# Kernel tuning notes

Hardware: AMD Instinct MI355X
Metric: run time of the kernel (lower is better)

The kernel has to match this reference:

```python
import jax, jax.numpy as jnp
import numpy as np

DIM = 256
NUM_HEADS = 4
HEAD_DIM = DIM // NUM_HEADS


def setup_inputs() -> dict:
    key = jax.random.key(0)
    ks = jax.random.split(key, 8)
    B, N, C = 4, 2048, DIM
    x = jax.random.normal(ks[0], (B, N, C), dtype=jnp.float32)
    R = jax.random.normal(ks[1], (B, 3, 3), dtype=jnp.float32)
    P = jax.random.normal(ks[2], (N, 3), dtype=jnp.float32)
    s = 1.0 / np.sqrt(C)
    qkv_w = jax.random.normal(ks[3], (3 * C, C), dtype=jnp.float32) * s
    qkv_b = jax.random.normal(ks[4], (3 * C,), dtype=jnp.float32) * 0.02
    proj_w = jax.random.normal(ks[5], (C, C), dtype=jnp.float32) * s
    proj_b = jax.random.normal(ks[6], (C,), dtype=jnp.float32) * 0.02
    pos_scale = jnp.asarray(1.0, dtype=jnp.float32)
    return {"x": x, "R": R, "P": P, "qkv_w": qkv_w, "qkv_b": qkv_b,
            "proj_w": proj_w, "proj_b": proj_b, "pos_scale": pos_scale}


def reference(x, R, P, qkv_w, qkv_b, proj_w, proj_b, pos_scale):
    B, N, C = x.shape
    H, D = NUM_HEADS, HEAD_DIM
    scale = D ** -0.5
    # qkv: (B,N,3C) -> (3,B,H,N,D)
    qkv = (x @ qkv_w.T + qkv_b).reshape(B, N, 3, H, D).transpose(2, 0, 3, 1, 4)
    q, k, v = qkv[0], qkv[1], qkv[2]
    # attention logits (B,H,N,N)
    attn = jnp.einsum('bhid,bhjd->bhij', q, k) * scale
    # positional bias: RP = (R @ P^T)^T -> (B,N,3); bias_ij = dot(RP_i, P_j)
    RP = jnp.einsum('bab,jb->bja', R, P) if False else jnp.einsum('bca,ja->bjc', jnp.swapaxes(R, 1, 2), P)
    RP = jnp.einsum('bcd,jd->bjc', R, P)  # (B,N,3): (R @ P.T).T
    bias = jnp.einsum('bik,jk->bij', RP, P)[:, None, :, :] * pos_scale  # (B,1,N,N) broadcast over heads
    attn = jax.nn.softmax(attn + bias, axis=-1)
    out = jnp.einsum('bhij,bhjd->bhid', attn, v)  # (B,H,N,D)
    out = out.transpose(0, 2, 1, 3).reshape(B, N, C)
    out = out @ proj_w.T + proj_b
    return out
```

## Files before the change

kernel.cpp:

```cpp
#include <hip/hip_runtime.h>
#include <hip/hip_bf16.h>

#define B_ 4
#define N_ 2048
#define C_ 256
#define H_ 4
#define D_ 64

typedef __attribute__((ext_vector_type(8))) short bf16x8;
typedef __attribute__((ext_vector_type(4))) float f32x4;

#define LOG2E 1.4426950408889634f

static __device__ inline unsigned short f2bf(float f) {
    unsigned u = __builtin_bit_cast(unsigned, f);
    unsigned r = (u + 0x7fffu + ((u >> 16) & 1u)) >> 16;
    return (unsigned short)r;
}
static __device__ inline float bf2f(unsigned short h) {
    unsigned u = ((unsigned)h) << 16;
    return __builtin_bit_cast(float, u);
}
static __device__ inline unsigned pack2(float a, float b) {
    __hip_bfloat162 h = __float22bfloat162_rn(make_float2(a, b));
    unsigned u;
    __builtin_memcpy(&u, &h, 4);
    return u;
}
static __device__ inline bf16x8 ld_frag(const unsigned short* p) {
    return __builtin_bit_cast(bf16x8, *(const uint4*)p);
}
static __device__ inline void gload_lds16(const unsigned short* g, unsigned short* l) {
    __builtin_amdgcn_global_load_lds(
        (const __attribute__((address_space(1))) unsigned int*)(g),
        (__attribute__((address_space(3))) unsigned int*)(l),
        16, 0, 0);
}
template<int CTRL>
static __device__ inline float fmax_dpp(float x) {
    int yi = __builtin_amdgcn_update_dpp(0, __builtin_bit_cast(int, x),
                                         CTRL, 0xf, 0xf, true);
    return fmaxf(x, __builtin_bit_cast(float, yi));
}

__global__ __launch_bounds__(256) void cvt_kernel(
    const float* __restrict__ x, const float* __restrict__ qkv_w,
    const float* __restrict__ proj_w, const float* __restrict__ Pm,
    unsigned short* __restrict__ xb, unsigned short* __restrict__ wqb,
    unsigned short* __restrict__ wpb, unsigned short* __restrict__ eb)
{
    const int bid = blockIdx.x, tid = threadIdx.x;
    if (bid >= 1152) {
        const int n = (bid - 1152) * 256 + tid;
        const float* pp = Pm + n * 3;
        float p0 = pp[0], p1 = pp[1], p2 = pp[2];
        unsigned u0 = f2bf(p0), u1 = f2bf(p1), u2 = f2bf(p2);
        unsigned v0 = f2bf(p0 - bf2f((unsigned short)u0));
        unsigned v1 = f2bf(p1 - bf2f((unsigned short)u1));
        unsigned v2 = f2bf(p2 - bf2f((unsigned short)u2));
        uint4 lo, hi;
        lo.x = u0 | (u1 << 16); lo.y = u2 | (v0 << 16);
        lo.z = v1 | (v2 << 16); lo.w = u0 | (u1 << 16);
        hi.x = u2; hi.y = 0u; hi.z = 0u; hi.w = 0u;
        *(uint4*)&eb[n * 16 + 0] = lo;
        *(uint4*)&eb[n * 16 + 8] = hi;
        return;
    }
    const float* s; unsigned short* d; int i;
    if (bid < 1024)      { s = x;      d = xb;  i = (bid * 256 + tid) * 8; }
    else if (bid < 1120) { s = qkv_w;  d = wqb; i = ((bid - 1024) * 256 + tid) * 8; }
    else                 { s = proj_w; d = wpb; i = ((bid - 1120) * 256 + tid) * 8; }
    float4 a = *(const float4*)(s + i);
    float4 b = *(const float4*)(s + i + 4);
    uint4 u;
    u.x = pack2(a.x, a.y); u.y = pack2(a.z, a.w);
    u.z = pack2(b.x, b.y); u.w = pack2(b.z, b.w);
    *(uint4*)(d + i) = u;
}

__global__ __launch_bounds__(256) void qkv_gemm(
    const unsigned short* __restrict__ xb, const unsigned short* __restrict__ wb,
    const float* __restrict__ bias, unsigned short* __restrict__ qb,
    unsigned short* __restrict__ kb, unsigned short* __restrict__ vt)
{
    __shared__ __align__(16) unsigned short As[128 * 40];
    __shared__ __align__(16) unsigned short Bs[128 * 40];
    const int m0 = blockIdx.x * 128, o0 = blockIdx.y * 128;
    const int tid = threadIdx.x;
    const int wave = tid >> 6, lane = tid & 63, quad = lane >> 4, l16 = lane & 15;
    const int wy = wave >> 1, wx = wave & 1;

    f32x4 acc[4][4];
    #pragma unroll
    for (int i = 0; i < 4; ++i)
        #pragma unroll
        for (int j = 0; j < 4; ++j) acc[i][j] = (f32x4){0.f, 0.f, 0.f, 0.f};

    const int srow = tid >> 1, soff = (tid & 1) * 16;

    for (int k0 = 0; k0 < 256; k0 += 32) {
        __syncthreads();
        {
            const unsigned short* sa = &xb[(size_t)(m0 + srow) * 256 + k0 + soff];
            const unsigned short* sb = &wb[(size_t)(o0 + srow) * 256 + k0 + soff];
            *(uint4*)&As[srow * 40 + soff + 0] = *(const uint4*)(sa + 0);
            *(uint4*)&As[srow * 40 + soff + 8] = *(const uint4*)(sa + 8);
            *(uint4*)&Bs[srow * 40 + soff + 0] = *(const uint4*)(sb + 0);
            *(uint4*)&Bs[srow * 40 + soff + 8] = *(const uint4*)(sb + 8);
        }
        __syncthreads();
        bf16x8 a[4], b[4];
        #pragma unroll
        for (int mt = 0; mt < 4; ++mt) a[mt] = ld_frag(&As[(wy * 64 + mt * 16 + l16) * 40 + quad * 8]);
        #pragma unroll
        for (int nt = 0; nt < 4; ++nt) b[nt] = ld_frag(&Bs[(wx * 64 + nt * 16 + l16) * 40 + quad * 8]);
        #pragma unroll
        for (int mt = 0; mt < 4; ++mt)
            #pragma unroll
            for (int nt = 0; nt < 4; ++nt)
                acc[mt][nt] = __builtin_amdgcn_mfma_f32_16x16x32_bf16(a[mt], b[nt], acc[mt][nt], 0, 0, 0);
    }

    const int sec = o0 + wx * 64;
    const int three = sec >> 8;
    const int h = (sec >> 6) & 3;
    const int b = m0 >> 11;
    float bv[4];
    #pragma unroll
    for (int nt = 0; nt < 4; ++nt) bv[nt] = bias[sec + nt * 16 + l16];

    if (three == 2) {
        const int n64 = (m0 + wy * 64) & 2047;
        const size_t bh64 = ((size_t)b * H_ + h) * 64;
        #pragma unroll
        for (int nt = 0; nt < 4; ++nt) {
            int d = nt * 16 + l16;
            #pragma unroll
            for (int r = 0; r < 4; ++r) {
                ushort4 v;
                v.x = f2bf(acc[0][nt][r] + bv[nt]);
                v.y = f2bf(acc[1][nt][r] + bv[nt]);
                v.z = f2bf(acc[2][nt][r] + bv[nt]);
                v.w = f2bf(acc[3][nt][r] + bv[nt]);
                *(ushort4*)&vt[(bh64 + d) * N_ + n64 + 16 * quad + 4 * r] = v;
            }
        }
    } else {
        unsigned short* dst = (three == 0) ? qb : kb;
        float sc = (three == 0) ? (0.125f * LOG2E) : 1.0f;
        #pragma unroll
        for (int mt = 0; mt < 4; ++mt)
            #pragma unroll
            for (int r = 0; r < 4; ++r) {
                int n = (m0 + wy * 64 + mt * 16 + quad * 4 + r) & 2047;
                size_t rowbase = (((size_t)b * H_ + h) * N_ + n) * D_;
                #pragma unroll
                for (int nt = 0; nt < 4; ++nt)
                    dst[rowbase + nt * 16 + l16] = f2bf((acc[mt][nt][r] + bv[nt]) * sc);
            }
    }
}

#define LDK 64

__global__ __launch_bounds__(256) void attn_kernel(
    const unsigned short* __restrict__ qb, const unsigned short* __restrict__ kb,
    const unsigned short* __restrict__ vt, const unsigned short* __restrict__ eb,
    const float* __restrict__ Rm, const float* __restrict__ Pm,
    const float* __restrict__ ps_ptr,
    unsigned short* __restrict__ Opart, float* __restrict__ ml)
{
    __shared__ __align__(16) unsigned short Ks[2][64 * LDK];
    __shared__ __align__(16) unsigned short Vs[64 * LDK];
    __shared__ __align__(16) unsigned short Ps[64 * LDK];

    const int bh = blockIdx.y;
    const int b = bh >> 2;
    const int i0 = blockIdx.x * 64;
    const int split = blockIdx.z;
    const int tid = threadIdx.x;
    const int wave = tid >> 6, lane = tid & 63;
    const int quad = lane >> 4, l16 = lane & 15;
    const int x7 = l16 & 7;
    const float ps = ps_ptr[0];

    const size_t base = (size_t)bh * N_ * D_;
    const unsigned short* qg = qb + base;
    const unsigned short* kg = kb + base;
    const unsigned short* vg = vt + base;

    const int jbeg = split * (N_ / 4);
    const int NT = (N_ / 4) / 64;

    const int rl = lane >> 3, sl = lane & 7;
    const int swz = (sl ^ rl) * 8;
    const unsigned short* kq = kg + (size_t)(jbeg + wave * 16 + rl) * D_ + swz;
    const unsigned short* vq = vg + (size_t)(wave * 16 + rl) * N_ + jbeg + swz;
    const unsigned short* ep = eb + (size_t)(jbeg + l16) * 16 + (quad & 1) * 8;

    {
        unsigned short* kd = &Ks[0][(wave * 16) * LDK];
        gload_lds16(kq,          kd);
        gload_lds16(kq + 8 * D_, kd + 8 * LDK);
        kq += 64 * D_;
    }
    bf16x8 ereg[4];
    #pragma unroll
    for (int t = 0; t < 4; ++t) ereg[t] = ld_frag(ep + t * 256);
    ep += 64 * 16;

    const int qrow = i0 + wave * 16 + l16;
    bf16x8 aq[3];
    #pragma unroll
    for (int ks = 0; ks < 2; ++ks)
        aq[ks] = ld_frag(&qg[(size_t)qrow * D_ + ks * 32 + quad * 8]);

    {
        float p0 = Pm[qrow * 3 + 0], p1 = Pm[qrow * 3 + 1], p2 = Pm[qrow * 3 + 2];
        float sc = ps * LOG2E;
        unsigned short ah[3], al[3];
        #pragma unroll
        for (int c = 0; c < 3; ++c) {
            float a = (Rm[b * 9 + c * 3 + 0] * p0 + Rm[b * 9 + c * 3 + 1] * p1
                     + Rm[b * 9 + c * 3 + 2] * p2) * sc;
            ah[c] = f2bf(a);
            al[c] = f2bf(a - bf2f(ah[c]));
        }
        bf16x8 e = (bf16x8){0,0,0,0,0,0,0,0};
        if (quad == 0) {
            e[0] = (short)ah[0]; e[1] = (short)ah[1]; e[2] = (short)ah[2];
            e[3] = (short)ah[0]; e[4] = (short)ah[1]; e[5] = (short)ah[2];
            e[6] = (short)al[0]; e[7] = (short)al[1];
        } else if (quad == 1) {
            e[0] = (short)al[2];
        }
        aq[2] = e;
    }

    const bf16x8 ones = (bf16x8){0x3F80,0x3F80,0x3F80,0x3F80,0x3F80,0x3F80,0x3F80,0x3F80};

    float m_run = -1e30f;
    f32x4 o_acc[4], lacc;
    #pragma unroll
    for (int t = 0; t < 4; ++t) o_acc[t] = (f32x4){0.f, 0.f, 0.f, 0.f};
    lacc = (f32x4){0.f, 0.f, 0.f, 0.f};

    for (int jt = 0; jt < NT; ++jt) {
        const int cur = jt & 1;
        const bool more = (jt + 1 < NT);

        asm volatile("s_waitcnt vmcnt(0)" ::: "memory");
        __builtin_amdgcn_s_barrier();
        __builtin_amdgcn_sched_barrier(0);

        bf16x8 enext[4];
        if (more) {
            #pragma unroll
            for (int t = 0; t < 4; ++t) enext[t] = ld_frag(ep + t * 256);
            ep += 64 * 16;
        }
        {
            unsigned short* vd = &Vs[(wave * 16) * LDK];
            gload_lds16(vq,          vd);
            gload_lds16(vq + 8 * N_, vd + 8 * LDK);
            vq += 64;
        }
        if (more) {
            unsigned short* kd = &Ks[cur ^ 1][(wave * 16) * LDK];
            gload_lds16(kq,          kd);
            gload_lds16(kq + 8 * D_, kd + 8 * LDK);
            kq += 64 * D_;
        }
        __builtin_amdgcn_sched_barrier(0);

        f32x4 s[4];
        __builtin_amdgcn_s_setprio(1);
        #pragma unroll
        for (int t = 0; t < 4; ++t) {
            const int rb = (l16 + 16 * t) * LDK;
            f32x4 c = {0.f, 0.f, 0.f, 0.f};
            #pragma unroll
            for (int ks = 0; ks < 2; ++ks) {
                bf16x8 bk = ld_frag(&Ks[cur][rb + (((ks * 4 + quad) ^ x7) * 8)]);
                c = __builtin_amdgcn_mfma_f32_16x16x32_bf16(aq[ks], bk, c, 0, 0, 0);
            }
            c = __builtin_amdgcn_mfma_f32_16x16x32_bf16(aq[2], ereg[t], c, 0, 0, 0);
            s[t] = c;
        }
        __builtin_amdgcn_s_setprio(0);
        if (more) {
            #pragma unroll
            for (int t = 0; t < 4; ++t) ereg[t] = enext[t];
        }

        float mt[4];
        #pragma unroll
        for (int t = 0; t < 4; ++t)
            mt[t] = fmaxf(fmaxf(s[t][0], s[t][1]), fmaxf(s[t][2], s[t][3]));
        float mx = fmaxf(fmaxf(mt[0], mt[1]), fmaxf(mt[2], mt[3]));
        mx = fmax_dpp<0xB1>(mx);
        mx = fmax_dpp<0x4E>(mx);
        mx = fmax_dpp<0x124>(mx);
        mx = fmax_dpp<0x128>(mx);

        if (__any(mx > m_run + 8.0f)) {
            float mnew = fmaxf(m_run, mx);
            float alpha = exp2f(m_run - mnew);
            #pragma unroll
            for (int t = 0; t < 4; ++t)
                #pragma unroll
                for (int r = 0; r < 4; ++r)
                    o_acc[t][r] *= alpha;
            #pragma unroll
            for (int r = 0; r < 4; ++r) lacc[r] *= alpha;
            m_run = mnew;
        }

        #pragma unroll
        for (int r = 0; r < 4; ++r) {
            float p0 = exp2f(s[0][r] - m_run), p1 = exp2f(s[1][r] - m_run);
            float p2 = exp2f(s[2][r] - m_run), p3 = exp2f(s[3][r] - m_run);
            uint2 w;
            w.x = pack2(p0, p1);
            w.y = pack2(p2, p3);
            const int prow = quad * 4 + r;
            *(uint2*)&Ps[(wave * 16 + prow) * LDK
                         + (((l16 >> 1) ^ (prow & 7)) * 8) + (l16 & 1) * 4] = w;
        }

        if (more) asm volatile("s_waitcnt vmcnt(2)" ::: "memory");
        else      asm volatile("s_waitcnt vmcnt(0)" ::: "memory");
        __builtin_amdgcn_s_barrier();
        __builtin_amdgcn_sched_barrier(0);

        __builtin_amdgcn_s_setprio(1);
        #pragma unroll
        for (int ks = 0; ks < 2; ++ks) {
            bf16x8 ap = ld_frag(&Ps[(wave * 16 + l16) * LDK
                                    + (((ks * 4 + quad) ^ x7) * 8)]);
            #pragma unroll
            for (int t = 0; t < 4; ++t) {
                bf16x8 bv = ld_frag(&Vs[(l16 + 16 * t) * LDK
                                        + (((ks * 4 + quad) ^ x7) * 8)]);
                o_acc[t] = __builtin_amdgcn_mfma_f32_16x16x32_bf16(ap, bv, o_acc[t], 0, 0, 0);
            }
            lacc = __builtin_amdgcn_mfma_f32_16x16x32_bf16(ap, ones, lacc, 0, 0, 0);
        }
        __builtin_amdgcn_s_setprio(0);
    }

    const size_t pbase = (size_t)(split * 16 + bh) * N_;
    #pragma unroll
    for (int r = 0; r < 4; ++r) {
        int row = i0 + wave * 16 + quad * 4 + r;
        #pragma unroll
        for (int t = 0; t < 4; ++t)
            Opart[(pbase + row) * D_ + l16 + 16 * t] = f2bf(o_acc[t][r]);
        if (l16 == 0) {
            float2* mlp = (float2*)ml;
            mlp[pbase + row] = make_float2(m_run, lacc[r]);
        }
    }
}

__global__ __launch_bounds__(256) void proj_gemm(
    const unsigned short* __restrict__ Opart, const float* __restrict__ ml,
    const unsigned short* __restrict__ wb, const float* __restrict__ bias,
    float* __restrict__ out)
{
    __shared__ __align__(16) unsigned short As[64 * 40];
    __shared__ __align__(16) unsigned short Bs[64 * 40];
    const int m0 = blockIdx.x * 64, o0 = blockIdx.y * 64;
    const int tid = threadIdx.x;
    const int wave = tid >> 6, lane = tid & 63, quad = lane >> 4, l16 = lane & 15;
    const float2* mlp = (const float2*)ml;

    const int srow = tid >> 2, scb = (tid & 3) * 8;
    const int sm = m0 + srow, sb = sm >> 11, sn = sm & 2047;

    float wgt[4][4];
    #pragma unroll
    for (int h = 0; h < 4; ++h) {
        size_t r1 = (size_t)(sb * 4 + h) * N_ + sn;
        float2 m0v = mlp[r1], m1v = mlp[r1 + 16 * N_];
        float2 m2v = mlp[r1 + 32 * N_], m3v = mlp[r1 + 48 * N_];
        float mm = fmaxf(fmaxf(m0v.x, m1v.x), fmaxf(m2v.x, m3v.x));
        float w0 = exp2f(m0v.x - mm), w1 = exp2f(m1v.x - mm);
        float w2 = exp2f(m2v.x - mm), w3 = exp2f(m3v.x - mm);
        float inv = 1.f / (m0v.y * w0 + m1v.y * w1 + m2v.y * w2 + m3v.y * w3);
        wgt[h][0] = w0 * inv; wgt[h][1] = w1 * inv;
        wgt[h][2] = w2 * inv; wgt[h][3] = w3 * inv;
    }

    f32x4 acc[4];
    #pragma unroll
    for (int j = 0; j < 4; ++j) acc[j] = (f32x4){0.f, 0.f, 0.f, 0.f};

    for (int k0 = 0; k0 < 256; k0 += 32) {
        const int h = k0 >> 6;
        const int d0 = (k0 & 63) + scb;
        __syncthreads();
        {
            size_t r1 = (size_t)(sb * 4 + h) * N_ + sn;
            union { uint4 u; unsigned short s[8]; } a0, a1, a2, a3;
            a0.u = *(const uint4*)&Opart[(r1 +  0 * N_) * D_ + d0];
            a1.u = *(const uint4*)&Opart[(r1 + 16 * N_) * D_ + d0];
            a2.u = *(const uint4*)&Opart[(r1 + 32 * N_) * D_ + d0];
            a3.u = *(const uint4*)&Opart[(r1 + 48 * N_) * D_ + d0];
            float w0 = wgt[h][0], w1 = wgt[h][1], w2 = wgt[h][2], w3 = wgt[h][3];
            uint4 mv;
            unsigned* mp = (unsigned*)&mv;
            #pragma unroll
            for (int j = 0; j < 4; ++j) {
                float lo = bf2f(a0.s[2*j]) * w0 + bf2f(a1.s[2*j]) * w1
                         + bf2f(a2.s[2*j]) * w2 + bf2f(a3.s[2*j]) * w3;
                float hi = bf2f(a0.s[2*j+1]) * w0 + bf2f(a1.s[2*j+1]) * w1
                         + bf2f(a2.s[2*j+1]) * w2 + bf2f(a3.s[2*j+1]) * w3;
                mp[j] = pack2(lo, hi);
            }
            *(uint4*)&As[srow * 40 + scb] = mv;
            *(uint4*)&Bs[srow * 40 + scb] = *(const uint4*)&wb[(size_t)(o0 + srow) * 256 + k0 + scb];
        }
        __syncthreads();
        bf16x8 a = ld_frag(&As[(wave * 16 + l16) * 40 + quad * 8]);
        #pragma unroll
        for (int nt = 0; nt < 4; ++nt) {
            bf16x8 b = ld_frag(&Bs[(nt * 16 + l16) * 40 + quad * 8]);
            acc[nt] = __builtin_amdgcn_mfma_f32_16x16x32_bf16(a, b, acc[nt], 0, 0, 0);
        }
    }

    float bv[4];
    #pragma unroll
    for (int nt = 0; nt < 4; ++nt) bv[nt] = bias[o0 + nt * 16 + l16];
    #pragma unroll
    for (int r = 0; r < 4; ++r) {
        int m = m0 + wave * 16 + quad * 4 + r;
        #pragma unroll
        for (int nt = 0; nt < 4; ++nt)
            out[(size_t)m * 256 + o0 + nt * 16 + l16] = acc[nt][r] + bv[nt];
    }
}

extern "C" void kernel_launch(void* const* d_in, const int* in_sizes, int n_in,
                              void* d_out, int out_size, void* d_ws, size_t ws_size,
                              hipStream_t stream) {
    const float* x       = (const float*)d_in[0];
    const float* Rm      = (const float*)d_in[1];
    const float* Pm      = (const float*)d_in[2];
    const float* qkv_w   = (const float*)d_in[3];
    const float* qkv_b   = (const float*)d_in[4];
    const float* proj_w  = (const float*)d_in[5];
    const float* proj_b  = (const float*)d_in[6];
    const float* pos_scl = (const float*)d_in[7];
    float* out = (float*)d_out;

    const size_t NE = (size_t)B_ * H_ * N_ * D_;
    unsigned short* opart = (unsigned short*)d_ws;
    unsigned short* qb    = opart + 4 * NE;
    unsigned short* kb    = qb   + NE;
    unsigned short* vtb   = kb   + NE;
    float*          mlb   = (float*)(vtb + NE);
    unsigned short* eb    = (unsigned short*)(mlb + (size_t)4 * 16 * N_ * 2);
    unsigned short* wqb   = eb  + 2048 * 16;
    unsigned short* wpb   = wqb + 768 * 256;
    unsigned short* xb    = opart;

    cvt_kernel<<<1160, 256, 0, stream>>>(x, qkv_w, proj_w, Pm, xb, wqb, wpb, eb);
    qkv_gemm<<<dim3(64, 6), 256, 0, stream>>>(xb, wqb, qkv_b, qb, kb, vtb);
    attn_kernel<<<dim3(32, 16, 4), 256, 0, stream>>>(qb, kb, vtb, eb, Rm, Pm, pos_scl, opart, mlb);
    proj_gemm<<<dim3(128, 4), 256, 0, stream>>>(opart, mlb, wpb, proj_b, out);
}
```

Baseline: 143.8 us.

## Software-pipeline attention loop: overlap softmax of previous tile with next QK^T

Restructures the flash-attention inner loop so each step computes the softmax and P·V of the previous key tile while issuing QK^T MFMAs for the current tile. V is double-buffered in LDS, and each iteration now has one barrier instead of two. The loop is manually unrolled by two with ping-pong score and bias-fragment registers, plus a prologue and epilogue. The aim is to hide exp/softmax latency and the extra barrier behind MFMA work, at the cost of higher register pressure and more LDS.

```diff
diff --git a/kernel.cpp b/kernel.cpp
--- a/kernel.cpp
+++ b/kernel.cpp
@@ -171,7 +171,7 @@
     unsigned short* __restrict__ Opart, float* __restrict__ ml)
 {
     __shared__ __align__(16) unsigned short Ks[2][64 * LDK];
-    __shared__ __align__(16) unsigned short Vs[64 * LDK];
+    __shared__ __align__(16) unsigned short Vs[2][64 * LDK];
     __shared__ __align__(16) unsigned short Ps[64 * LDK];
 
     const int bh = blockIdx.y;
@@ -190,7 +190,6 @@
     const unsigned short* vg = vt + base;
 
     const int jbeg = split * (N_ / 4);
-    const int NT = (N_ / 4) / 64;
 
     const int rl = lane >> 3, sl = lane & 7;
     const int swz = (sl ^ rl) * 8;
@@ -198,16 +197,27 @@
     const unsigned short* vq = vg + (size_t)(wave * 16 + rl) * N_ + jbeg + swz;
     const unsigned short* ep = eb + (size_t)(jbeg + l16) * 16 + (quad & 1) * 8;
 
-    {
-        unsigned short* kd = &Ks[0][(wave * 16) * LDK];
+    auto ISSUE_K = [&](int nb) {
+        unsigned short* kd = &Ks[nb][(wave * 16) * LDK];
         gload_lds16(kq,          kd);
         gload_lds16(kq + 8 * D_, kd + 8 * LDK);
         kq += 64 * D_;
-    }
-    bf16x8 ereg[4];
-    #pragma unroll
-    for (int t = 0; t < 4; ++t) ereg[t] = ld_frag(ep + t * 256);
-    ep += 64 * 16;
+    };
+    auto ISSUE_V = [&](int nb) {
+        unsigned short* vd = &Vs[nb][(wave * 16) * LDK];
+        gload_lds16(vq,          vd);
+        gload_lds16(vq + 8 * N_, vd + 8 * LDK);
+        vq += 64;
+    };
+    auto LOAD_E = [&](bf16x8 (&e)[4]) {
+        #pragma unroll
+        for (int t = 0; t < 4; ++t) e[t] = ld_frag(ep + t * 256);
+        ep += 64 * 16;
+    };
+
+    ISSUE_K(0);
+    bf16x8 eA[4], eB[4];
+    LOAD_E(eA);
 
     const int qrow = i0 + wave * 16 + l16;
     bf16x8 aq[3];
@@ -245,35 +255,9 @@
     for (int t = 0; t < 4; ++t) o_acc[t] = (f32x4){0.f, 0.f, 0.f, 0.f};
     lacc = (f32x4){0.f, 0.f, 0.f, 0.f};
 
-    for (int jt = 0; jt < NT; ++jt) {
-        const int cur = jt & 1;
-        const bool more = (jt + 1 < NT);
-
-        asm volatile("s_waitcnt vmcnt(0)" ::: "memory");
-        __builtin_amdgcn_s_barrier();
-        __builtin_amdgcn_sched_barrier(0);
-
-        bf16x8 enext[4];
-        if (more) {
-            #pragma unroll
-            for (int t = 0; t < 4; ++t) enext[t] = ld_frag(ep + t * 256);
-            ep += 64 * 16;
-        }
-        {
-            unsigned short* vd = &Vs[(wave * 16) * LDK];
-            gload_lds16(vq,          vd);
-            gload_lds16(vq + 8 * N_, vd + 8 * LDK);
-            vq += 64;
-        }
-        if (more) {
-            unsigned short* kd = &Ks[cur ^ 1][(wave * 16) * LDK];
-            gload_lds16(kq,          kd);
-            gload_lds16(kq + 8 * D_, kd + 8 * LDK);
-            kq += 64 * D_;
-        }
-        __builtin_amdgcn_sched_barrier(0);
-
-        f32x4 s[4];
+    f32x4 sA[4], sB[4];
+
+    auto S_COMPUTE = [&](f32x4 (&sc)[4], int kb_, bf16x8 (&ec)[4]) {
         __builtin_amdgcn_s_setprio(1);
         #pragma unroll
         for (int t = 0; t < 4; ++t) {
@@ -281,18 +265,16 @@
             f32x4 c = {0.f, 0.f, 0.f, 0.f};
             #pragma unroll
             for (int ks = 0; ks < 2; ++ks) {
-                bf16x8 bk = ld_frag(&Ks[cur][rb + (((ks * 4 + quad) ^ x7) * 8)]);
+                bf16x8 bk = ld_frag(&Ks[kb_][rb + (((ks * 4 + quad) ^ x7) * 8)]);
                 c = __builtin_amdgcn_mfma_f32_16x16x32_bf16(aq[ks], bk, c, 0, 0, 0);
             }
-            c = __builtin_amdgcn_mfma_f32_16x16x32_bf16(aq[2], ereg[t], c, 0, 0, 0);
-            s[t] = c;
+            c = __builtin_amdgcn_mfma_f32_16x16x32_bf16(aq[2], ec[t], c, 0, 0, 0);
+            sc[t] = c;
         }
         __builtin_amdgcn_s_setprio(0);
-        if (more) {
-            #pragma unroll
-            for (int t = 0; t < 4; ++t) ereg[t] = enext[t];
-        }
-
+    };
+
+    auto SOFTMAX = [&](f32x4 (&s)[4]) {
         float mt[4];
         #pragma unroll
         for (int t = 0; t < 4; ++t)
@@ -302,7 +284,6 @@
         mx = fmax_dpp<0x4E>(mx);
         mx = fmax_dpp<0x124>(mx);
         mx = fmax_dpp<0x128>(mx);
-
         if (__any(mx > m_run + 8.0f)) {
             float mnew = fmaxf(m_run, mx);
             float alpha = exp2f(m_run - mnew);
@@ -315,7 +296,6 @@
             for (int r = 0; r < 4; ++r) lacc[r] *= alpha;
             m_run = mnew;
         }
-
         #pragma unroll
         for (int r = 0; r < 4; ++r) {
             float p0 = exp2f(s[0][r] - m_run), p1 = exp2f(s[1][r] - m_run);
@@ -327,12 +307,9 @@
             *(uint2*)&Ps[(wave * 16 + prow) * LDK
                          + (((l16 >> 1) ^ (prow & 7)) * 8) + (l16 & 1) * 4] = w;
         }
-
-        if (more) asm volatile("s_waitcnt vmcnt(2)" ::: "memory");
-        else      asm volatile("s_waitcnt vmcnt(0)" ::: "memory");
-        __builtin_amdgcn_s_barrier();
-        __builtin_amdgcn_sched_barrier(0);
-
+    };
+
+    auto PV = [&](int vb_) {
         __builtin_amdgcn_s_setprio(1);
         #pragma unroll
         for (int ks = 0; ks < 2; ++ks) {
@@ -340,14 +317,48 @@
                                     + (((ks * 4 + quad) ^ x7) * 8)]);
             #pragma unroll
             for (int t = 0; t < 4; ++t) {
-                bf16x8 bv = ld_frag(&Vs[(l16 + 16 * t) * LDK
-                                        + (((ks * 4 + quad) ^ x7) * 8)]);
+                bf16x8 bv = ld_frag(&Vs[vb_][(l16 + 16 * t) * LDK
+                                             + (((ks * 4 + quad) ^ x7) * 8)]);
                 o_acc[t] = __builtin_amdgcn_mfma_f32_16x16x32_bf16(ap, bv, o_acc[t], 0, 0, 0);
             }
             lacc = __builtin_amdgcn_mfma_f32_16x16x32_bf16(ap, ones, lacc, 0, 0, 0);
         }
         __builtin_amdgcn_s_setprio(0);
-    }
+    };
+
+    auto STEP = [&](int cur, bool more, f32x4 (&snew)[4], f32x4 (&sold)[4],
+                    bf16x8 (&euse)[4], bf16x8 (&eload)[4]) {
+        asm volatile("s_waitcnt vmcnt(0)" ::: "memory");
+        __builtin_amdgcn_s_barrier();
+        __builtin_amdgcn_sched_barrier(0);
+        if (more) ISSUE_K(cur ^ 1);
+        ISSUE_V(cur);
+        SOFTMAX(sold);
+        S_COMPUTE(snew, cur, euse);
+        if (more) LOAD_E(eload);
+        PV(cur ^ 1);
+    };
+
+    asm volatile("s_waitcnt vmcnt(0)" ::: "memory");
+    __builtin_amdgcn_s_barrier();
+    __builtin_amdgcn_sched_barrier(0);
+    ISSUE_K(1);
+    ISSUE_V(0);
+    S_COMPUTE(sA, 0, eA);
+    LOAD_E(eB);
+
+    #pragma unroll 1
+    for (int it = 0; it < 3; ++it) {
+        STEP(1, true, sB, sA, eB, eA);
+        STEP(0, true, sA, sB, eA, eB);
+    }
+    STEP(1, false, sB, sA, eB, eA);
+
+    asm volatile("s_waitcnt vmcnt(0)" ::: "memory");
+    __builtin_amdgcn_s_barrier();
+    __builtin_amdgcn_sched_barrier(0);
+    SOFTMAX(sB);
+    PV(1);
 
     const size_t pbase = (size_t)(split * 16 + bh) * N_;
     #pragma unroll
```

Result: faster. 136.2 us (-5.3%).
